# Performance work log

Hardware: AMD Instinct MI355X
Metric: run time of the kernel (lower is better)

## Reference

```python
import jax, jax.numpy as jnp
import numpy as np

B, L, D = 8, 4096, 512
H, DK = 8, 64           # num_heads, key_dim = D // H
SAMPLE_K = 512
CONV_K = 3
POOL = 2


def setup_inputs() -> dict:
    key = jax.random.key(0)
    ks = jax.random.split(key, 8)
    x = jax.random.normal(ks[0], (B, L, D), dtype=jnp.float32)
    sample_indices = jax.random.randint(ks[1], (SAMPLE_K,), 0, L, dtype=jnp.int32)
    s = 1.0 / np.sqrt(D)
    Wq = jax.random.uniform(ks[2], (D, H * DK), jnp.float32, -s, s)
    Wk = jax.random.uniform(ks[3], (D, H * DK), jnp.float32, -s, s)
    Wv = jax.random.uniform(ks[4], (D, H * DK), jnp.float32, -s, s)
    conv_w = jax.random.normal(ks[5], (CONV_K, H * DK, H * DK), jnp.float32) * 0.02
    conv_b = jnp.zeros((H * DK,), jnp.float32)
    comb_w = jax.random.normal(ks[6], (H * DK, D), jnp.float32) * 0.02
    comb_b = jnp.zeros((D,), jnp.float32)
    return {"x": x, "Wq": Wq, "Wk": Wk, "Wv": Wv, "conv_w": conv_w,
            "conv_b": conv_b, "comb_w": comb_w, "comb_b": comb_b,
            "sample_indices": sample_indices}


def reference(x, Wq, Wk, Wv, conv_w, conv_b, comb_w, comb_b, sample_indices):
    b, l, _ = x.shape
    # QKV projections -> [B, H, L, DK]
    Q = (x @ Wq).reshape(b, l, H, DK).transpose(0, 2, 1, 3)
    K = (x @ Wk).reshape(b, l, H, DK).transpose(0, 2, 1, 3)
    V = (x @ Wv).reshape(b, l, H, DK).transpose(0, 2, 1, 3)
    # sample K/V along sequence axis -> [B, H, S, DK]
    Ks = jnp.take(K, sample_indices, axis=2)
    Vs = jnp.take(V, sample_indices, axis=2)
    # scores [B, H, L, S]
    scores = jnp.einsum('bhld,bhsd->bhls', Q, Ks) / jnp.sqrt(jnp.float32(DK))
    # second gather along the sampled axis (size S); indices in [0, L) so
    # out-of-range indices are clipped (JAX default), matching jit-safe semantics
    scores = jnp.take(scores, sample_indices, axis=3, mode='clip')
    attn = jax.nn.softmax(scores, axis=-1)
    out = jnp.einsum('bhls,bhsd->bhld', attn, Vs)          # [B, H, L, DK]
    out = out.transpose(0, 2, 1, 3).reshape(b, l, H * DK)  # [B, L, E]
    # Conv1D, padding SAME, NWC / WIO
    out = jax.lax.conv_general_dilated(
        out, conv_w, window_strides=(1,), padding='SAME',
        dimension_numbers=('NWC', 'WIO', 'NWC')) + conv_b
    out = jax.nn.elu(out)
    # MaxPool1D: pool == stride, L divisible by POOL
    out = out.reshape(b, l // POOL, POOL, H * DK).max(axis=2)
    # combine heads (Dense back to D); Dropout is identity at inference
    out = out @ comb_w + comb_b
    return out
```

## Files before the change

### kernel.cpp

```cpp
#include <hip/hip_runtime.h>


typedef __attribute__((ext_vector_type(8))) short  short8;
typedef __attribute__((ext_vector_type(4))) short  short4b;
typedef __attribute__((ext_vector_type(4))) float  f32x4;

#define LSEQ   4096
#define SK     512
#define EDIM   512
#define LPAD   4098
#define PADROW 2098176
#define SCALE2 0.180336880f

static __device__ __forceinline__ float bf2f(unsigned short h) {
    union { unsigned int u; float f; } v; v.u = ((unsigned int)h) << 16; return v.f;
}
static __device__ __forceinline__ unsigned short f2bf(float f) {
    union { float f; unsigned int u; } v; v.f = f;
    unsigned int r = (v.u + 0x7fffu + ((v.u >> 16) & 1u)) >> 16;
    return (unsigned short)r;
}
static __device__ __forceinline__ unsigned int cvt_pk_bf16(float lo, float hi) {
    unsigned int r;
    asm("v_cvt_pk_bf16_f32 %0, %1, %2" : "=v"(r) : "v"(lo), "v"(hi));
    return r;
}
typedef __attribute__((address_space(1))) const unsigned int  gu32;
typedef __attribute__((address_space(3))) unsigned int        lu32;
static __device__ __forceinline__ void g2l16(const unsigned short* g, unsigned short* l)
{
    __builtin_amdgcn_global_load_lds((gu32*)g, (lu32*)l, 16, 0, 0);
}

__global__ __launch_bounds__(256)
void cvt_bf16(const float* __restrict__ src, unsigned short* __restrict__ dst)
{
    const size_t i = ((size_t)blockIdx.x * 256 + threadIdx.x) * 8;
    const float4 a = *(const float4*)(src + i);
    const float4 b = *(const float4*)(src + i + 4);
    short8 o;
    o[0] = (short)f2bf(a.x); o[1] = (short)f2bf(a.y);
    o[2] = (short)f2bf(a.z); o[3] = (short)f2bf(a.w);
    o[4] = (short)f2bf(b.x); o[5] = (short)f2bf(b.y);
    o[6] = (short)f2bf(b.z); o[7] = (short)f2bf(b.w);
    *(short8*)(dst + i) = o;
}

__global__ __launch_bounds__(256)
void tr_f32_bf16(unsigned short* __restrict__ dst, const float* __restrict__ src,
                 int R, int C)
{
    __shared__ unsigned short T[64][72];
    const int t  = threadIdx.x;
    const int r0 = blockIdx.y * 64, c0 = blockIdx.x * 64;
    const int row = t >> 2, cg = (t & 3) * 16;
    const float* s = src + (size_t)(r0 + row) * C + c0 + cg;
    const float4 f0 = *(const float4*)s;
    const float4 f1 = *(const float4*)(s + 4);
    const float4 f2 = *(const float4*)(s + 8);
    const float4 f3 = *(const float4*)(s + 12);
    T[row][cg + 0]  = f2bf(f0.x); T[row][cg + 1]  = f2bf(f0.y);
    T[row][cg + 2]  = f2bf(f0.z); T[row][cg + 3]  = f2bf(f0.w);
    T[row][cg + 4]  = f2bf(f1.x); T[row][cg + 5]  = f2bf(f1.y);
    T[row][cg + 6]  = f2bf(f1.z); T[row][cg + 7]  = f2bf(f1.w);
    T[row][cg + 8]  = f2bf(f2.x); T[row][cg + 9]  = f2bf(f2.y);
    T[row][cg + 10] = f2bf(f2.z); T[row][cg + 11] = f2bf(f2.w);
    T[row][cg + 12] = f2bf(f3.x); T[row][cg + 13] = f2bf(f3.y);
    T[row][cg + 14] = f2bf(f3.z); T[row][cg + 15] = f2bf(f3.w);
    __syncthreads();
    unsigned short* d = dst + (size_t)(c0 + row) * R + r0 + cg;
    short8 o0, o1;
    #pragma unroll
    for (int k = 0; k < 8; ++k) o0[k] = (short)T[cg + k][row];
    #pragma unroll
    for (int k = 0; k < 8; ++k) o1[k] = (short)T[cg + 8 + k][row];
    *(short8*)d       = o0;
    *(short8*)(d + 8) = o1;
}

__global__ __launch_bounds__(256)
void tr_bf16(unsigned short* __restrict__ dst, const unsigned short* __restrict__ src,
             int R, int C)
{
    __shared__ unsigned short T[64][72];
    const size_t bofs = (size_t)blockIdx.z * (size_t)R * (size_t)C;
    src += bofs; dst += bofs;
    const int t  = threadIdx.x;
    const int r0 = blockIdx.y * 64, c0 = blockIdx.x * 64;
    const int row = t >> 2, cg = (t & 3) * 16;
    const unsigned short* s = src + (size_t)(r0 + row) * C + c0 + cg;
    *(short8*)&T[row][cg]     = *(const short8*)s;
    *(short8*)&T[row][cg + 8] = *(const short8*)(s + 8);
    __syncthreads();
    unsigned short* d = dst + (size_t)(c0 + row) * R + r0 + cg;
    short8 o0, o1;
    #pragma unroll
    for (int k = 0; k < 8; ++k) o0[k] = (short)T[cg + k][row];
    #pragma unroll
    for (int k = 0; k < 8; ++k) o1[k] = (short)T[cg + 8 + k][row];
    *(short8*)d       = o0;
    *(short8*)(d + 8) = o1;
}

__global__ __launch_bounds__(256)
void gather_rows(const unsigned short* __restrict__ xb, const int* __restrict__ sidx,
                 unsigned short* __restrict__ xkg, unsigned short* __restrict__ xvg)
{
    const int blk = blockIdx.x;
    const int b = blk >> 9, j = blk & 511;
    const int t = threadIdx.x;
    int qv = sidx[j];               qv = qv < 0 ? 0 : (qv > LSEQ - 1 ? LSEQ - 1 : qv);
    int cv = qv < SK - 1 ? qv : SK - 1;
    int pv = sidx[cv];              pv = pv < 0 ? 0 : (pv > LSEQ - 1 ? LSEQ - 1 : pv);
    const unsigned int* xs = (const unsigned int*)xb;
    unsigned int* kd = (unsigned int*)xkg;
    unsigned int* vd = (unsigned int*)xvg;
    const size_t dst = ((size_t)b * SK + j) * 256 + t;
    kd[dst] = xs[((size_t)b * LSEQ + pv) * 256 + t];
    vd[dst] = xs[((size_t)b * LSEQ + qv) * 256 + t];
}

__global__ __launch_bounds__(256)
void zero_pad(unsigned short* __restrict__ attpad)
{
    const int i = blockIdx.x * 256 + threadIdx.x;
    const int b = i >> 9, c = i & 511;
    attpad[(size_t)b * PADROW + c] = 0;
    attpad[(size_t)b * PADROW + (size_t)(LPAD - 1) * 512 + c] = 0;
}

template<int MODE>
__global__ __launch_bounds__(256)
void gemm128(const unsigned short* __restrict__ A, const unsigned short* __restrict__ Bt,
             const float* __restrict__ bias, void* __restrict__ Cout, int K)
{
    __shared__ unsigned short As[2][128 * 32];
    __shared__ unsigned short Bs[2][128 * 32];
    const int t    = threadIdx.x;
    const int n0   = blockIdx.x * 128;
    const int m0   = blockIdx.y * 128;
    const int lane = t & 63, wv = t >> 6;
    const int q = lane >> 4, ln = lane & 15;
    const int wm = (wv & 1) * 64, wn = (wv >> 1) * 64;

    const int srl = (wv << 5) + (lane >> 2);
    const int scs = (lane & 3) * 8;
    const unsigned short* arow0;
    const unsigned short* arow1;
    if (MODE == 1) {
        const int gr0 = m0 + srl;
        arow0 = A + (size_t)(gr0 >> 12) * PADROW + (size_t)(gr0 & 4095) * 512 + scs;
        arow1 = arow0 + (size_t)16 * 512;
    } else {
        arow0 = A + (size_t)(m0 + srl) * K + scs;
        arow1 = arow0 + (size_t)16 * K;
    }
    const unsigned short* brow0 = Bt + (size_t)(n0 + srl) * K + scs;
    const unsigned short* brow1 = brow0 + (size_t)16 * K;

    const int lb0 = (wv << 5) * 32;
    const int lb1 = lb0 + 16 * 32;

    const f32x4 zero = {0.f, 0.f, 0.f, 0.f};
    f32x4 acc[4][4];
    #pragma unroll
    for (int i = 0; i < 4; ++i)
        #pragma unroll
        for (int j = 0; j < 4; ++j) acc[i][j] = zero;

    g2l16(arow0, &As[0][lb0]);  g2l16(arow1, &As[0][lb1]);
    g2l16(brow0, &Bs[0][lb0]);  g2l16(brow1, &Bs[0][lb1]);

    for (int k0 = 0; k0 < K; k0 += 32) {
        const int cur = (k0 >> 5) & 1;
        __syncthreads();
        if (k0 + 32 < K) {
            const int nxt = cur ^ 1;
            g2l16(arow0 + k0 + 32, &As[nxt][lb0]);
            g2l16(arow1 + k0 + 32, &As[nxt][lb1]);
            g2l16(brow0 + k0 + 32, &Bs[nxt][lb0]);
            g2l16(brow1 + k0 + 32, &Bs[nxt][lb1]);
        }
        short8 af[4], bf[4];
        #pragma unroll
        for (int mt = 0; mt < 4; ++mt)
            af[mt] = *(const short8*)&As[cur][(wm + mt * 16 + ln) * 32 + q * 8];
        #pragma unroll
        for (int nt = 0; nt < 4; ++nt)
            bf[nt] = *(const short8*)&Bs[cur][(wn + nt * 16 + ln) * 32 + q * 8];
        #pragma unroll
        for (int mt = 0; mt < 4; ++mt)
            #pragma unroll
            for (int nt = 0; nt < 4; ++nt)
                acc[mt][nt] = __builtin_amdgcn_mfma_f32_16x16x32_bf16(af[mt], bf[nt], acc[mt][nt], 0, 0, 0);
    }

    if (MODE == 0) {
        unsigned short* C = (unsigned short*)Cout;
        #pragma unroll
        for (int mt = 0; mt < 4; ++mt)
            #pragma unroll
            for (int r = 0; r < 4; ++r) {
                const int grow = m0 + wm + mt * 16 + q * 4 + r;
                unsigned short* cp = C + (size_t)grow * 512 + n0 + wn + ln;
                #pragma unroll
                for (int nt = 0; nt < 4; ++nt) cp[nt * 16] = f2bf(acc[mt][nt][r]);
            }
    } else if (MODE == 2) {
        float* C = (float*)Cout;
        float bb[4];
        #pragma unroll
        for (int nt = 0; nt < 4; ++nt) bb[nt] = bias[n0 + wn + nt * 16 + ln];
        #pragma unroll
        for (int mt = 0; mt < 4; ++mt)
            #pragma unroll
            for (int r = 0; r < 4; ++r) {
                const int grow = m0 + wm + mt * 16 + q * 4 + r;
                float* cp = C + (size_t)grow * 512 + n0 + wn + ln;
                #pragma unroll
                for (int nt = 0; nt < 4; ++nt) cp[nt * 16] = acc[mt][nt][r] + bb[nt];
            }
    } else {
        unsigned short* C = (unsigned short*)Cout;
        float bb[4];
        #pragma unroll
        for (int nt = 0; nt < 4; ++nt) bb[nt] = bias[n0 + wn + nt * 16 + ln];
        #pragma unroll
        for (int mt = 0; mt < 4; ++mt) {
            const int grow = m0 + wm + mt * 16 + q * 4;
            const int b = grow >> 12, l = grow & 4095;
            unsigned short* cp = C + ((size_t)b * 2048 + (l >> 1)) * 512 + n0 + wn + ln;
            #pragma unroll
            for (int nt = 0; nt < 4; ++nt) {
                float v0 = acc[mt][nt][0] + bb[nt]; v0 = v0 > 0.f ? v0 : __expf(v0) - 1.f;
                float v1 = acc[mt][nt][1] + bb[nt]; v1 = v1 > 0.f ? v1 : __expf(v1) - 1.f;
                float v2 = acc[mt][nt][2] + bb[nt]; v2 = v2 > 0.f ? v2 : __expf(v2) - 1.f;
                float v3 = acc[mt][nt][3] + bb[nt]; v3 = v3 > 0.f ? v3 : __expf(v3) - 1.f;
                cp[nt * 16]       = f2bf(fmaxf(v0, v1));
                cp[512 + nt * 16] = f2bf(fmaxf(v2, v3));
            }
        }
    }
}

__global__ __launch_bounds__(256, 2)
void attn_fused(const unsigned short* __restrict__ xb, const unsigned short* __restrict__ WqT,
                const unsigned short* __restrict__ Kg, const unsigned short* __restrict__ Vt,
                unsigned short* __restrict__ attpad)
{
    __shared__ unsigned short Ks[128][72];
    __shared__ unsigned short Vs[64][136];
    __shared__ unsigned short Pp[128][136];
    const int t = threadIdx.x;
    const int wv = t >> 6, lane = t & 63, q = lane >> 4, ln = lane & 15;
    const int l0 = blockIdx.x * 128, h = blockIdx.y, b = blockIdx.z;
    const int qr0 = wv * 32;
    const f32x4 zero = {0.f, 0.f, 0.f, 0.f};

    const unsigned short* kgb = Kg + (size_t)b * SK * 512 + h * 64;
    const unsigned short* vtb = Vt + ((size_t)(b * EDIM + h * 64)) * SK;
    const int ksr = t >> 1, ksc = (t & 1) * 32;
    const int vsr = t >> 2, vsc = (t & 3) * 32;

    short8 kp0, kp1, kp2, kp3, vp0, vp1, vp2, vp3;
    {
        const unsigned short* ks = kgb + (size_t)ksr * 512 + ksc;
        kp0 = *(const short8*)ks;        kp1 = *(const short8*)(ks + 8);
        kp2 = *(const short8*)(ks + 16); kp3 = *(const short8*)(ks + 24);
        const unsigned short* vs = vtb + (size_t)vsr * SK + vsc;
        vp0 = *(const short8*)vs;        vp1 = *(const short8*)(vs + 8);
        vp2 = *(const short8*)(vs + 16); vp3 = *(const short8*)(vs + 24);
    }

    f32x4 qacc[2][4];
    #pragma unroll
    for (int g = 0; g < 2; ++g)
        #pragma unroll
        for (int nt = 0; nt < 4; ++nt) qacc[g][nt] = zero;
    const unsigned short* xr0 = xb + ((size_t)(b * LSEQ + l0 + qr0 + ln)) * 512 + q * 8;
    const unsigned short* xr1 = xr0 + (size_t)16 * 512;
    const unsigned short* wqp = WqT + ((size_t)(h * 64 + ln)) * 512 + q * 8;
    for (int ks = 0; ks < 16; ++ks) {
        const short8 ax0 = *(const short8*)(xr0 + ks * 32);
        const short8 ax1 = *(const short8*)(xr1 + ks * 32);
        #pragma unroll
        for (int nt = 0; nt < 4; ++nt) {
            const short8 bw = *(const short8*)(wqp + nt * 16 * 512 + ks * 32);
            qacc[0][nt] = __builtin_amdgcn_mfma_f32_16x16x32_bf16(ax0, bw, qacc[0][nt], 0, 0, 0);
            qacc[1][nt] = __builtin_amdgcn_mfma_f32_16x16x32_bf16(ax1, bw, qacc[1][nt], 0, 0, 0);
        }
    }
    #pragma unroll
    for (int g = 0; g < 2; ++g)
        #pragma unroll
        for (int nt = 0; nt < 4; ++nt)
            #pragma unroll
            for (int r = 0; r < 4; ++r)
                Pp[qr0 + g * 16 + q * 4 + r][nt * 16 + ln] = f2bf(qacc[g][nt][r]);
    asm volatile("s_waitcnt lgkmcnt(0)" ::: "memory");
    short8 bq[2][2];
    #pragma unroll
    for (int g = 0; g < 2; ++g) {
        bq[g][0] = *(const short8*)&Pp[qr0 + g * 16 + ln][q * 8];
        bq[g][1] = *(const short8*)&Pp[qr0 + g * 16 + ln][q * 8 + 32];
    }

    float m_run[2] = {-1e30f, -1e30f}, l_run[2] = {0.f, 0.f};
    f32x4 o[2][4];
    #pragma unroll
    for (int g = 0; g < 2; ++g)
        #pragma unroll
        for (int j = 0; j < 4; ++j) o[g][j] = zero;

    for (int c = 0; c < 4; ++c) {
        *(short8*)&Ks[ksr][ksc]      = kp0;  *(short8*)&Ks[ksr][ksc + 8]  = kp1;
        *(short8*)&Ks[ksr][ksc + 16] = kp2;  *(short8*)&Ks[ksr][ksc + 24] = kp3;
        *(short8*)&Vs[vsr][vsc]      = vp0;  *(short8*)&Vs[vsr][vsc + 8]  = vp1;
        *(short8*)&Vs[vsr][vsc + 16] = vp2;  *(short8*)&Vs[vsr][vsc + 24] = vp3;
        __syncthreads();

        f32x4 st[8][2];
        #pragma unroll
        for (int mt = 0; mt < 8; ++mt) {
            const short8 ak0 = *(const short8*)&Ks[mt * 16 + ln][q * 8];
            const short8 ak1 = *(const short8*)&Ks[mt * 16 + ln][q * 8 + 32];
            #pragma unroll
            for (int g = 0; g < 2; ++g) {
                f32x4 a = zero;
                a = __builtin_amdgcn_mfma_f32_16x16x32_bf16(ak0, bq[g][0], a, 0, 0, 0);
                a = __builtin_amdgcn_mfma_f32_16x16x32_bf16(ak1, bq[g][1], a, 0, 0, 0);
                #pragma unroll
                for (int r = 0; r < 4; ++r) a[r] *= SCALE2;
                st[mt][g] = a;
            }
        }

        float alpha_[2];
        #pragma unroll
        for (int g = 0; g < 2; ++g) {
            float mx = st[0][g][0];
            #pragma unroll
            for (int mt = 0; mt < 8; ++mt)
                #pragma unroll
                for (int r = 0; r < 4; ++r) mx = fmaxf(mx, st[mt][g][r]);
            mx = fmaxf(mx, __shfl_xor(mx, 16));
            mx = fmaxf(mx, __shfl_xor(mx, 32));
            const float m_new = fmaxf(m_run[g], mx);
            alpha_[g] = __builtin_amdgcn_exp2f(m_run[g] - m_new);
            m_run[g] = m_new;
            float ls = 0.f;
            #pragma unroll
            for (int mt = 0; mt < 8; ++mt) {
                const float p0 = __builtin_amdgcn_exp2f(st[mt][g][0] - m_new);
                const float p1 = __builtin_amdgcn_exp2f(st[mt][g][1] - m_new);
                const float p2 = __builtin_amdgcn_exp2f(st[mt][g][2] - m_new);
                const float p3 = __builtin_amdgcn_exp2f(st[mt][g][3] - m_new);
                ls += (p0 + p1) + (p2 + p3);
                uint2 pw;
                pw.x = cvt_pk_bf16(p0, p1);
                pw.y = cvt_pk_bf16(p2, p3);
                *(uint2*)&Pp[qr0 + g * 16 + ln][mt * 16 + q * 4] = pw;
            }
            ls += __shfl_xor(ls, 16);
            ls += __shfl_xor(ls, 32);
            l_run[g] = l_run[g] * alpha_[g] + ls;
        }

        #pragma unroll
        for (int g = 0; g < 2; ++g) {
            #pragma unroll
            for (int r = 0; r < 4; ++r) {
                const float ab = __shfl(alpha_[g], q * 4 + r);
                #pragma unroll
                for (int j = 0; j < 4; ++j) o[g][j][r] *= ab;
            }
        }

        if (c < 3) {
            const unsigned short* ks = kgb + (size_t)((c + 1) * 128 + ksr) * 512 + ksc;
            kp0 = *(const short8*)ks;        kp1 = *(const short8*)(ks + 8);
            kp2 = *(const short8*)(ks + 16); kp3 = *(const short8*)(ks + 24);
            const unsigned short* vs = vtb + (size_t)vsr * SK + (c + 1) * 128 + vsc;
            vp0 = *(const short8*)vs;        vp1 = *(const short8*)(vs + 8);
            vp2 = *(const short8*)(vs + 16); vp3 = *(const short8*)(vs + 24);
        }

        asm volatile("s_waitcnt lgkmcnt(0)" ::: "memory");

        #pragma unroll
        for (int ks2 = 0; ks2 < 4; ++ks2) {
            const short8 ap0 = *(const short8*)&Pp[qr0 + ln][ks2 * 32 + q * 8];
            const short8 ap1 = *(const short8*)&Pp[qr0 + 16 + ln][ks2 * 32 + q * 8];
            #pragma unroll
            for (int j = 0; j < 4; ++j) {
                const short8 bv = *(const short8*)&Vs[j * 16 + ln][ks2 * 32 + q * 8];
                o[0][j] = __builtin_amdgcn_mfma_f32_16x16x32_bf16(ap0, bv, o[0][j], 0, 0, 0);
                o[1][j] = __builtin_amdgcn_mfma_f32_16x16x32_bf16(ap1, bv, o[1][j], 0, 0, 0);
            }
        }
        __syncthreads();
    }

    #pragma unroll
    for (int g = 0; g < 2; ++g) {
        const float li = 1.f / l_run[g];
        #pragma unroll
        for (int r = 0; r < 4; ++r) {
            const float ib = __shfl(li, q * 4 + r);
            const int rl = qr0 + g * 16 + q * 4 + r;
            #pragma unroll
            for (int j = 0; j < 4; ++j)
                attpad[((size_t)b * PADROW) + (size_t)(l0 + rl + 1) * 512 + h * 64 + j * 16 + ln]
                    = f2bf(o[g][j][r] * ib);
        }
    }
}

extern "C" void kernel_launch(void* const* d_in, const int* in_sizes, int n_in,
                              void* d_out, int out_size, void* d_ws, size_t ws_size,
                              hipStream_t stream)
{
    const float* x    = (const float*)d_in[0];
    const float* Wq   = (const float*)d_in[1];
    const float* Wk   = (const float*)d_in[2];
    const float* Wv   = (const float*)d_in[3];
    const float* cw   = (const float*)d_in[4];
    const float* cb   = (const float*)d_in[5];
    const float* mw   = (const float*)d_in[6];
    const float* mb2  = (const float*)d_in[7];
    const int*   sidx = (const int*)d_in[8];
    float* out = (float*)d_out;

    char* ws = (char*)d_ws;
    unsigned short* xb    = (unsigned short*)(ws + 0);
    unsigned short* Pool  = (unsigned short*)(ws + 0);
    unsigned short* Pad   = (unsigned short*)(ws + 33554432);
    unsigned short* xkg   = (unsigned short*)(ws + 33554432);
    unsigned short* xvg   = (unsigned short*)(ws + 37748736);
    unsigned short* Vg    = (unsigned short*)(ws + 41943040);
    unsigned short* Kg    = (unsigned short*)(ws + 67125248);
    unsigned short* Vt    = (unsigned short*)(ws + 71319552);
    unsigned short* WqT   = (unsigned short*)(ws + 75513856);
    unsigned short* WkT   = (unsigned short*)(ws + 76038144);
    unsigned short* WvT   = (unsigned short*)(ws + 76562432);
    unsigned short* CombT = (unsigned short*)(ws + 77086720);
    unsigned short* ConvT = (unsigned short*)(ws + 77611008);

    dim3 blk(256);

    cvt_bf16<<<dim3(8192), blk, 0, stream>>>(x, xb);

    tr_f32_bf16<<<dim3(8, 8),  blk, 0, stream>>>(WqT,   Wq, 512, 512);
    tr_f32_bf16<<<dim3(8, 8),  blk, 0, stream>>>(WkT,   Wk, 512, 512);
    tr_f32_bf16<<<dim3(8, 8),  blk, 0, stream>>>(WvT,   Wv, 512, 512);
    tr_f32_bf16<<<dim3(8, 8),  blk, 0, stream>>>(CombT, mw, 512, 512);
    tr_f32_bf16<<<dim3(8, 24), blk, 0, stream>>>(ConvT, cw, 1536, 512);

    gather_rows<<<dim3(4096), blk, 0, stream>>>(xb, sidx, xkg, xvg);

    gemm128<0><<<dim3(4, 32), blk, 0, stream>>>(xkg, WkT, nullptr, Kg, 512);
    gemm128<0><<<dim3(4, 32), blk, 0, stream>>>(xvg, WvT, nullptr, Vg, 512);

    tr_bf16<<<dim3(8, 8, 8), blk, 0, stream>>>(Vt, Vg, 512, 512);

    zero_pad<<<dim3(16), blk, 0, stream>>>(Pad);
    attn_fused<<<dim3(32, 8, 8), blk, 0, stream>>>(xb, WqT, Kg, Vt, Pad);

    gemm128<1><<<dim3(4, 256), blk, 0, stream>>>(Pad, ConvT, cb, Pool, 1536);

    gemm128<2><<<dim3(4, 128), blk, 0, stream>>>(Pool, CombT, mb2, out, 512);
}
```

Before: 381.6 us.

## Use 128x256 tile GEMM with XCD-aware block mapping for conv stage

```diff
diff --git a/kernel.cpp b/kernel.cpp
--- a/kernel.cpp
+++ b/kernel.cpp
@@ -145,16 +145,8 @@
 
     const int srl = (wv << 5) + (lane >> 2);
     const int scs = (lane & 3) * 8;
-    const unsigned short* arow0;
-    const unsigned short* arow1;
-    if (MODE == 1) {
-        const int gr0 = m0 + srl;
-        arow0 = A + (size_t)(gr0 >> 12) * PADROW + (size_t)(gr0 & 4095) * 512 + scs;
-        arow1 = arow0 + (size_t)16 * 512;
-    } else {
-        arow0 = A + (size_t)(m0 + srl) * K + scs;
-        arow1 = arow0 + (size_t)16 * K;
-    }
+    const unsigned short* arow0 = A + (size_t)(m0 + srl) * K + scs;
+    const unsigned short* arow1 = arow0 + (size_t)16 * K;
     const unsigned short* brow0 = Bt + (size_t)(n0 + srl) * K + scs;
     const unsigned short* brow1 = brow0 + (size_t)16 * K;
 
@@ -206,7 +198,7 @@
                 #pragma unroll
                 for (int nt = 0; nt < 4; ++nt) cp[nt * 16] = f2bf(acc[mt][nt][r]);
             }
-    } else if (MODE == 2) {
+    } else {
         float* C = (float*)Cout;
         float bb[4];
         #pragma unroll
@@ -220,25 +212,93 @@
                 #pragma unroll
                 for (int nt = 0; nt < 4; ++nt) cp[nt * 16] = acc[mt][nt][r] + bb[nt];
             }
-    } else {
-        unsigned short* C = (unsigned short*)Cout;
-        float bb[4];
-        #pragma unroll
-        for (int nt = 0; nt < 4; ++nt) bb[nt] = bias[n0 + wn + nt * 16 + ln];
-        #pragma unroll
-        for (int mt = 0; mt < 4; ++mt) {
-            const int grow = m0 + wm + mt * 16 + q * 4;
-            const int b = grow >> 12, l = grow & 4095;
-            unsigned short* cp = C + ((size_t)b * 2048 + (l >> 1)) * 512 + n0 + wn + ln;
-            #pragma unroll
-            for (int nt = 0; nt < 4; ++nt) {
-                float v0 = acc[mt][nt][0] + bb[nt]; v0 = v0 > 0.f ? v0 : __expf(v0) - 1.f;
-                float v1 = acc[mt][nt][1] + bb[nt]; v1 = v1 > 0.f ? v1 : __expf(v1) - 1.f;
-                float v2 = acc[mt][nt][2] + bb[nt]; v2 = v2 > 0.f ? v2 : __expf(v2) - 1.f;
-                float v3 = acc[mt][nt][3] + bb[nt]; v3 = v3 > 0.f ? v3 : __expf(v3) - 1.f;
-                cp[nt * 16]       = f2bf(fmaxf(v0, v1));
-                cp[512 + nt * 16] = f2bf(fmaxf(v2, v3));
-            }
+    }
+}
+
+__global__ __launch_bounds__(256)
+void gemm256n(const unsigned short* __restrict__ A, const unsigned short* __restrict__ Bt,
+              const float* __restrict__ bias, unsigned short* __restrict__ Cout, int K)
+{
+    __shared__ unsigned short As[2][128 * 32];
+    __shared__ unsigned short Bs[2][256 * 32];
+    const int t    = threadIdx.x;
+    const int bid  = blockIdx.x;
+    const int mi   = (bid & 7) * 32 + ((bid >> 3) >> 1);
+    const int ni   = (bid >> 3) & 1;
+    const int m0   = mi * 128;
+    const int n0   = ni * 256;
+    const int lane = t & 63, wv = t >> 6;
+    const int q = lane >> 4, ln = lane & 15;
+    const int wm = (wv & 1) * 64, wn = (wv >> 1) * 128;
+
+    const int srl = (wv << 5) + (lane >> 2);
+    const int scs = (lane & 3) * 8;
+    const int gr0 = m0 + srl;
+    const unsigned short* arow0 = A + (size_t)(gr0 >> 12) * PADROW + (size_t)(gr0 & 4095) * 512 + scs;
+    const unsigned short* arow1 = arow0 + (size_t)16 * 512;
+    const int brl = (wv << 6) + (lane >> 2);
+    const unsigned short* brow0 = Bt + (size_t)(n0 + brl) * K + scs;
+    const unsigned short* brow1 = brow0 + (size_t)16 * K;
+    const unsigned short* brow2 = brow0 + (size_t)32 * K;
+    const unsigned short* brow3 = brow0 + (size_t)48 * K;
+
+    const int alb0 = (wv << 5) * 32, alb1 = alb0 + 16 * 32;
+    const int blb0 = (wv << 6) * 32;
+    const int blb1 = blb0 + 16 * 32, blb2 = blb0 + 32 * 32, blb3 = blb0 + 48 * 32;
+
+    const f32x4 zero = {0.f, 0.f, 0.f, 0.f};
+    f32x4 acc[4][8];
+    #pragma unroll
+    for (int i = 0; i < 4; ++i)
+        #pragma unroll
+        for (int j = 0; j < 8; ++j) acc[i][j] = zero;
+
+    g2l16(arow0, &As[0][alb0]);  g2l16(arow1, &As[0][alb1]);
+    g2l16(brow0, &Bs[0][blb0]);  g2l16(brow1, &Bs[0][blb1]);
+    g2l16(brow2, &Bs[0][blb2]);  g2l16(brow3, &Bs[0][blb3]);
+
+    for (int k0 = 0; k0 < K; k0 += 32) {
+        const int cur = (k0 >> 5) & 1;
+        __syncthreads();
+        if (k0 + 32 < K) {
+            const int nxt = cur ^ 1;
+            g2l16(arow0 + k0 + 32, &As[nxt][alb0]);
+            g2l16(arow1 + k0 + 32, &As[nxt][alb1]);
+            g2l16(brow0 + k0 + 32, &Bs[nxt][blb0]);
+            g2l16(brow1 + k0 + 32, &Bs[nxt][blb1]);
+            g2l16(brow2 + k0 + 32, &Bs[nxt][blb2]);
+            g2l16(brow3 + k0 + 32, &Bs[nxt][blb3]);
+        }
+        short8 af[4], bf[8];
+        #pragma unroll
+        for (int mt = 0; mt < 4; ++mt)
+            af[mt] = *(const short8*)&As[cur][(wm + mt * 16 + ln) * 32 + q * 8];
+        #pragma unroll
+        for (int nt = 0; nt < 8; ++nt)
+            bf[nt] = *(const short8*)&Bs[cur][(wn + nt * 16 + ln) * 32 + q * 8];
+        #pragma unroll
+        for (int mt = 0; mt < 4; ++mt)
+            #pragma unroll
+            for (int nt = 0; nt < 8; ++nt)
+                acc[mt][nt] = __builtin_amdgcn_mfma_f32_16x16x32_bf16(af[mt], bf[nt], acc[mt][nt], 0, 0, 0);
+    }
+
+    float bb[8];
+    #pragma unroll
+    for (int nt = 0; nt < 8; ++nt) bb[nt] = bias[n0 + wn + nt * 16 + ln];
+    #pragma unroll
+    for (int mt = 0; mt < 4; ++mt) {
+        const int grow = m0 + wm + mt * 16 + q * 4;
+        const int b = grow >> 12, l = grow & 4095;
+        unsigned short* cp = Cout + ((size_t)b * 2048 + (l >> 1)) * 512 + n0 + wn + ln;
+        #pragma unroll
+        for (int nt = 0; nt < 8; ++nt) {
+            float v0 = acc[mt][nt][0] + bb[nt]; v0 = v0 > 0.f ? v0 : __expf(v0) - 1.f;
+            float v1 = acc[mt][nt][1] + bb[nt]; v1 = v1 > 0.f ? v1 : __expf(v1) - 1.f;
+            float v2 = acc[mt][nt][2] + bb[nt]; v2 = v2 > 0.f ? v2 : __expf(v2) - 1.f;
+            float v3 = acc[mt][nt][3] + bb[nt]; v3 = v3 > 0.f ? v3 : __expf(v3) - 1.f;
+            cp[nt * 16]       = f2bf(fmaxf(v0, v1));
+            cp[512 + nt * 16] = f2bf(fmaxf(v2, v3));
         }
     }
 }
@@ -466,7 +526,7 @@
     zero_pad<<<dim3(16), blk, 0, stream>>>(Pad);
     attn_fused<<<dim3(32, 8, 8), blk, 0, stream>>>(xb, WqT, Kg, Vt, Pad);
 
-    gemm128<1><<<dim3(4, 256), blk, 0, stream>>>(Pad, ConvT, cb, Pool, 1536);
+    gemm256n<<<dim3(512), blk, 0, stream>>>(Pad, ConvT, cb, Pool, 1536);
 
     gemm128<2><<<dim3(4, 128), blk, 0, stream>>>(Pool, CombT, mb2, out, 512);
 }
```

Result: slower. 398.1 us (+4.3%).
